# Performance work log

Measured on AMD Instinct MI355X. Metric: run time of the kernel, lower is better.

## Reference

```python
import math
import jax, jax.numpy as jnp
import numpy as np

B, L, S, H, E, D = 4, 2048, 2048, 8, 64, 64

def setup_inputs() -> dict:
    key = jax.random.key(0)
    kq, kk, kv = jax.random.split(key, 3)
    return {
        "queries": jax.random.normal(kq, (B, L, H, E), dtype=jnp.float32),
        "keys": jax.random.normal(kk, (B, S, H, E), dtype=jnp.float32),
        "values": jax.random.normal(kv, (B, S, H, D), dtype=jnp.float32),
    }

def reference(queries, keys, values):
    E_ = queries.shape[-1]
    scale = 1.0 / math.sqrt(E_)
    # scores: [B, H, L, S]
    scores = jnp.einsum('blhe,bshe->bhls', queries, keys)
    A = jax.nn.softmax(scale * scores, axis=-1)
    # dropout omitted (eval mode / p=0.0)
    out = jnp.einsum('bhls,bshd->blhd', A, values)
    return out
```

## Files before the change

### kernel.cpp

```cpp
#include <hip/hip_runtime.h>
#include <hip/hip_bf16.h>


#define BNUM 4
#define LLEN 2048
#define SLEN 2048
#define HNUM 8
#define EDIM 64

typedef __attribute__((ext_vector_type(8))) short bf16x8;
typedef __attribute__((ext_vector_type(4))) float f32x4;

__device__ __forceinline__ short f2bf(float f) {
    union { __hip_bfloat16 b; short s; } u;
    u.b = __float2bfloat16(f);
    return u.s;
}

#if __has_builtin(__builtin_amdgcn_global_load_lds)
#define HAVE_GLL 1
#else
#define HAVE_GLL 0
#endif

__device__ __forceinline__ void stage16(const short* g, short* l) {
#if HAVE_GLL
    __builtin_amdgcn_global_load_lds(
        (const __attribute__((address_space(1))) void*)g,
        (__attribute__((address_space(3))) void*)l, 16, 0, 0);
#else
    *(bf16x8*)l = *(const bf16x8*)g;
#endif
}

__global__ __launch_bounds__(256)
void prep(const float* __restrict__ Kg, const float* __restrict__ Vg,
          short* __restrict__ Kc, short* __restrict__ Vt)
{
    __shared__ short tile[EDIM][80];
    if (blockIdx.y == 0) {
        const int t = blockIdx.x * 256 + threadIdx.x;
        const int e8 = t & 7;
        const int tmp = t >> 3;
        const int h = tmp & 7;
        const int tmp2 = tmp >> 3;
        const int s = tmp2 & (SLEN - 1);
        const int b = tmp2 >> 11;
        const float4* src = (const float4*)(Kg + (((size_t)(b * SLEN + s) * HNUM + h) * EDIM + e8 * 8));
        float4 a = src[0], bb = src[1];
        bf16x8 o;
        o[0]=f2bf(a.x);  o[1]=f2bf(a.y);  o[2]=f2bf(a.z);  o[3]=f2bf(a.w);
        o[4]=f2bf(bb.x); o[5]=f2bf(bb.y); o[6]=f2bf(bb.z); o[7]=f2bf(bb.w);
        *(bf16x8*)(Kc + ((size_t)((b * HNUM + h) * SLEN + s) * EDIM + e8 * 8)) = o;
    } else {
        if (blockIdx.x >= 1024) return;
        const int x = blockIdx.x;
        const int s0 = (x & 31) * 64;
        const int bh = x >> 5;
        const int b = bh >> 3, h = bh & 7;
        {
            const int sr = threadIdx.x >> 2, dc = (threadIdx.x & 3) * 16;
            const float4* src = (const float4*)(Vg + (((size_t)(b * SLEN + s0 + sr) * HNUM + h) * EDIM + dc));
            #pragma unroll
            for (int j4 = 0; j4 < 4; ++j4) {
                float4 a = src[j4];
                tile[dc + j4*4 + 0][sr] = f2bf(a.x);
                tile[dc + j4*4 + 1][sr] = f2bf(a.y);
                tile[dc + j4*4 + 2][sr] = f2bf(a.z);
                tile[dc + j4*4 + 3][sr] = f2bf(a.w);
            }
        }
        __syncthreads();
        {
            const int dr = threadIdx.x >> 2, sc = (threadIdx.x & 3) * 16;
            short* dst = Vt + ((size_t)((b * HNUM + h) * EDIM + dr) * SLEN + s0 + sc);
            *(bf16x8*)dst       = *(const bf16x8*)&tile[dr][sc];
            *(bf16x8*)(dst + 8) = *(const bf16x8*)&tile[dr][sc + 8];
        }
    }
}

__global__ __launch_bounds__(256, 3)
void fa_fwd(const float* __restrict__ Qg, const short* __restrict__ Kc,
            const short* __restrict__ Vt, float* __restrict__ Og)
{
    __shared__ short sKV[16384];
    __shared__ float sL[4][64];

    const int tid  = threadIdx.x;
    const int wave = tid >> 6;
    const int lane = tid & 63;
    const int m    = lane & 15;
    const int quad = lane >> 4;
    const int h = blockIdx.y, b = blockIdx.z;
    const int qbase = blockIdx.x * 64;
    const int bh = b * HNUM + h;

    const short* Kbh = Kc + (size_t)bh * SLEN * EDIM;
    const short* Vbh = Vt + (size_t)bh * EDIM * SLEN;

    int ksrc[4], vsrc[4];
    short *kdst[4], *vdst[4];
    #pragma unroll
    for (int p = 0; p < 4; ++p) {
        const int krow = wave * 32 + p * 8 + (lane >> 3);
        const int kchk = (lane & 7) ^ ((p & 1) * 4 + ((lane >> 3) & 3));
        ksrc[p] = krow * EDIM + kchk * 8;
        kdst[p] = sKV + (wave * 256 + p * 64 + lane) * 8;
        const int vrow = p * 16 + (lane >> 2);
        const int vchk = (lane & 3) ^ ((lane >> 2) & 3);
        vsrc[p] = vrow * SLEN + wave * 32 + vchk * 8;
        vdst[p] = sKV + 8192 + (wave * 256 + p * 64 + lane) * 8;
    }

#define STAGE_TILE(s0)                                                  \
    do {                                                                \
        _Pragma("unroll")                                               \
        for (int p = 0; p < 4; ++p) {                                   \
            stage16(Kbh + (size_t)(s0) * EDIM + ksrc[p], kdst[p]);      \
            stage16(Vbh + (s0) + vsrc[p], vdst[p]);                     \
        }                                                               \
    } while (0)

    const float csc = 0.18033688011112042f;
    bf16x8 qfrag[4][2];
    #pragma unroll
    for (int qt = 0; qt < 4; ++qt)
        #pragma unroll
        for (int kb = 0; kb < 2; ++kb) {
            const float* qp = Qg + ((size_t)(b * LLEN + qbase + qt * 16 + m) * HNUM + h) * EDIM
                              + kb * 32 + quad * 8;
            float4 x0 = *(const float4*)qp;
            float4 x1 = *(const float4*)(qp + 4);
            bf16x8 f;
            f[0]=f2bf(x0.x*csc); f[1]=f2bf(x0.y*csc); f[2]=f2bf(x0.z*csc); f[3]=f2bf(x0.w*csc);
            f[4]=f2bf(x1.x*csc); f[5]=f2bf(x1.y*csc); f[6]=f2bf(x1.z*csc); f[7]=f2bf(x1.w*csc);
            qfrag[qt][kb] = f;
        }

    const int gk  = ((m >> 2) & 1) * 4 + (m & 3);
    const int pi0 = 8 * (m >> 2) + (m & 3);
    const int kOff00 = (wave * 32 + pi0)     * EDIM + ((quad)     ^ gk) * 8;
    const int kOff01 = (wave * 32 + pi0)     * EDIM + ((4 + quad) ^ gk) * 8;
    const int kOff10 = (wave * 32 + pi0 + 4) * EDIM + ((quad)     ^ gk) * 8;
    const int kOff11 = (wave * 32 + pi0 + 4) * EDIM + ((4 + quad) ^ gk) * 8;
    const int vOffB = 8192 + wave * 2048 + m * 32 + ((quad ^ (m & 3)) * 8);

    f32x4 oacc[4][4];
    #pragma unroll
    for (int i = 0; i < 4; ++i)
        #pragma unroll
        for (int j = 0; j < 4; ++j) oacc[i][j] = (f32x4){0.f, 0.f, 0.f, 0.f};
    float lsum[4] = {0.f, 0.f, 0.f, 0.f};

    STAGE_TILE(0);
    __syncthreads();

    for (int s0 = 0; s0 < SLEN; s0 += 128) {
        bf16x8 kf00 = *(const bf16x8*)(sKV + kOff00);
        bf16x8 kf01 = *(const bf16x8*)(sKV + kOff01);
        bf16x8 kf10 = *(const bf16x8*)(sKV + kOff10);
        bf16x8 kf11 = *(const bf16x8*)(sKV + kOff11);
        bf16x8 vf[4];
        #pragma unroll
        for (int dt = 0; dt < 4; ++dt)
            vf[dt] = *(const bf16x8*)(sKV + vOffB + dt * 512);

        __syncthreads();

        if (s0 + 128 < SLEN) STAGE_TILE(s0 + 128);

        #pragma unroll
        for (int qt = 0; qt < 4; ++qt) {
            f32x4 a0 = {0.f, 0.f, 0.f, 0.f};
            f32x4 a1 = {0.f, 0.f, 0.f, 0.f};
            a0 = __builtin_amdgcn_mfma_f32_16x16x32_bf16(kf00, qfrag[qt][0], a0, 0, 0, 0);
            a0 = __builtin_amdgcn_mfma_f32_16x16x32_bf16(kf01, qfrag[qt][1], a0, 0, 0, 0);
            a1 = __builtin_amdgcn_mfma_f32_16x16x32_bf16(kf10, qfrag[qt][0], a1, 0, 0, 0);
            a1 = __builtin_amdgcn_mfma_f32_16x16x32_bf16(kf11, qfrag[qt][1], a1, 0, 0, 0);
            float p0 = __builtin_amdgcn_exp2f(a0[0]);
            float p1 = __builtin_amdgcn_exp2f(a0[1]);
            float p2 = __builtin_amdgcn_exp2f(a0[2]);
            float p3 = __builtin_amdgcn_exp2f(a0[3]);
            float p4 = __builtin_amdgcn_exp2f(a1[0]);
            float p5 = __builtin_amdgcn_exp2f(a1[1]);
            float p6 = __builtin_amdgcn_exp2f(a1[2]);
            float p7 = __builtin_amdgcn_exp2f(a1[3]);
            lsum[qt] += ((p0 + p1) + (p2 + p3)) + ((p4 + p5) + (p6 + p7));
            bf16x8 pf;
            pf[0]=f2bf(p0); pf[1]=f2bf(p1); pf[2]=f2bf(p2); pf[3]=f2bf(p3);
            pf[4]=f2bf(p4); pf[5]=f2bf(p5); pf[6]=f2bf(p6); pf[7]=f2bf(p7);
            #pragma unroll
            for (int dt = 0; dt < 4; ++dt)
                oacc[qt][dt] = __builtin_amdgcn_mfma_f32_16x16x32_bf16(pf, vf[dt], oacc[qt][dt], 0, 0, 0);
        }

        __syncthreads();
    }

    #pragma unroll
    for (int qt = 0; qt < 4; ++qt) {
        float l = lsum[qt];
        l += __shfl_xor(l, 16);
        l += __shfl_xor(l, 32);
        if (lane < 16) sL[wave][qt * 16 + lane] = l;
    }
    __syncthreads();

    float* sO = (float*)sKV;
    for (int w = 0; w < 4; ++w) {
        if (wave == w) {
            #pragma unroll
            for (int qt = 0; qt < 4; ++qt)
                #pragma unroll
                for (int dt = 0; dt < 4; ++dt)
                    #pragma unroll
                    for (int r = 0; r < 4; ++r) {
                        const int q = qt * 16 + quad * 4 + r;
                        const int d = dt * 16 + m;
                        if (w == 0) sO[q * 64 + d] = oacc[qt][dt][r];
                        else        sO[q * 64 + d] += oacc[qt][dt][r];
                    }
        }
        __syncthreads();
    }

    {
        const int q = tid >> 2;
        const int dcol = (tid & 3) * 16;
        const float l = sL[0][q] + sL[1][q] + sL[2][q] + sL[3][q];
        const float inv = 1.0f / l;
        float* orow = Og + ((size_t)(b * LLEN + qbase + q) * HNUM + h) * EDIM + dcol;
        #pragma unroll
        for (int j = 0; j < 4; ++j) {
            float4 v = *(const float4*)(sO + q * 64 + dcol + j * 4);
            v.x *= inv; v.y *= inv; v.z *= inv; v.w *= inv;
            *(float4*)(orow + j * 4) = v;
        }
    }
}

extern "C" void kernel_launch(void* const* d_in, const int* in_sizes, int n_in,
                              void* d_out, int out_size, void* d_ws, size_t ws_size,
                              hipStream_t stream) {
    const float* Q = (const float*)d_in[0];
    const float* K = (const float*)d_in[1];
    const float* V = (const float*)d_in[2];
    float* O = (float*)d_out;

    const size_t NE = (size_t)BNUM * LLEN * HNUM * EDIM;
    short* Kc = (short*)d_ws;
    short* Vt = Kc + NE;

    prep<<<dim3(2048, 2), dim3(256), 0, stream>>>(K, V, Kc, Vt);
    fa_fwd<<<dim3(LLEN / 64, HNUM, BNUM), dim3(256), 0, stream>>>(Q, Kc, Vt, O);
}
```

Baseline: 153.0 us.

## Load K/V fragments directly from global memory instead of staging through LDS

Removes the global_load_lds staging of K and V tiles into shared memory and the per-tile barriers; each wave now reads its MFMA fragments straight from global (L2-cached) memory. Shared memory is reduced to a padded output-reduction buffer, which allows raising the launch-bound occupancy hint from 3 to 4 blocks. The padding of the output buffer row stride aims to reduce bank conflicts. The trade-off is less coalesced global loads and exposed global latency, with no explicit prefetch of the next tile.

```diff
diff --git a/kernel.cpp b/kernel.cpp
--- a/kernel.cpp
+++ b/kernel.cpp
@@ -15,22 +15,6 @@
     union { __hip_bfloat16 b; short s; } u;
     u.b = __float2bfloat16(f);
     return u.s;
-}
-
-#if __has_builtin(__builtin_amdgcn_global_load_lds)
-#define HAVE_GLL 1
-#else
-#define HAVE_GLL 0
-#endif
-
-__device__ __forceinline__ void stage16(const short* g, short* l) {
-#if HAVE_GLL
-    __builtin_amdgcn_global_load_lds(
-        (const __attribute__((address_space(1))) void*)g,
-        (__attribute__((address_space(3))) void*)l, 16, 0, 0);
-#else
-    *(bf16x8*)l = *(const bf16x8*)g;
-#endif
 }
 
 __global__ __launch_bounds__(256)
@@ -80,11 +64,11 @@
     }
 }
 
-__global__ __launch_bounds__(256, 3)
+__global__ __launch_bounds__(256, 4)
 void fa_fwd(const float* __restrict__ Qg, const short* __restrict__ Kc,
             const short* __restrict__ Vt, float* __restrict__ Og)
 {
-    __shared__ short sKV[16384];
+    __shared__ float sO[64 * 68];
     __shared__ float sL[4][64];
 
     const int tid  = threadIdx.x;
@@ -98,29 +82,6 @@
 
     const short* Kbh = Kc + (size_t)bh * SLEN * EDIM;
     const short* Vbh = Vt + (size_t)bh * EDIM * SLEN;
-
-    int ksrc[4], vsrc[4];
-    short *kdst[4], *vdst[4];
-    #pragma unroll
-    for (int p = 0; p < 4; ++p) {
-        const int krow = wave * 32 + p * 8 + (lane >> 3);
-        const int kchk = (lane & 7) ^ ((p & 1) * 4 + ((lane >> 3) & 3));
-        ksrc[p] = krow * EDIM + kchk * 8;
-        kdst[p] = sKV + (wave * 256 + p * 64 + lane) * 8;
-        const int vrow = p * 16 + (lane >> 2);
-        const int vchk = (lane & 3) ^ ((lane >> 2) & 3);
-        vsrc[p] = vrow * SLEN + wave * 32 + vchk * 8;
-        vdst[p] = sKV + 8192 + (wave * 256 + p * 64 + lane) * 8;
-    }
-
-#define STAGE_TILE(s0)                                                  \
-    do {                                                                \
-        _Pragma("unroll")                                               \
-        for (int p = 0; p < 4; ++p) {                                   \
-            stage16(Kbh + (size_t)(s0) * EDIM + ksrc[p], kdst[p]);      \
-            stage16(Vbh + (s0) + vsrc[p], vdst[p]);                     \
-        }                                                               \
-    } while (0)
 
     const float csc = 0.18033688011112042f;
     bf16x8 qfrag[4][2];
@@ -138,13 +99,10 @@
             qfrag[qt][kb] = f;
         }
 
-    const int gk  = ((m >> 2) & 1) * 4 + (m & 3);
     const int pi0 = 8 * (m >> 2) + (m & 3);
-    const int kOff00 = (wave * 32 + pi0)     * EDIM + ((quad)     ^ gk) * 8;
-    const int kOff01 = (wave * 32 + pi0)     * EDIM + ((4 + quad) ^ gk) * 8;
-    const int kOff10 = (wave * 32 + pi0 + 4) * EDIM + ((quad)     ^ gk) * 8;
-    const int kOff11 = (wave * 32 + pi0 + 4) * EDIM + ((4 + quad) ^ gk) * 8;
-    const int vOffB = 8192 + wave * 2048 + m * 32 + ((quad ^ (m & 3)) * 8);
+    const short* kp0 = Kbh + (size_t)(wave * 32 + pi0) * EDIM + quad * 8;
+    const short* kp1 = kp0 + 4 * EDIM;
+    const short* vp0 = Vbh + (size_t)m * SLEN + wave * 32 + quad * 8;
 
     f32x4 oacc[4][4];
     #pragma unroll
@@ -153,22 +111,18 @@
         for (int j = 0; j < 4; ++j) oacc[i][j] = (f32x4){0.f, 0.f, 0.f, 0.f};
     float lsum[4] = {0.f, 0.f, 0.f, 0.f};
 
-    STAGE_TILE(0);
-    __syncthreads();
-
     for (int s0 = 0; s0 < SLEN; s0 += 128) {
-        bf16x8 kf00 = *(const bf16x8*)(sKV + kOff00);
-        bf16x8 kf01 = *(const bf16x8*)(sKV + kOff01);
-        bf16x8 kf10 = *(const bf16x8*)(sKV + kOff10);
-        bf16x8 kf11 = *(const bf16x8*)(sKV + kOff11);
-        bf16x8 vf[4];
-        #pragma unroll
-        for (int dt = 0; dt < 4; ++dt)
-            vf[dt] = *(const bf16x8*)(sKV + vOffB + dt * 512);
-
-        __syncthreads();
-
-        if (s0 + 128 < SLEN) STAGE_TILE(s0 + 128);
+        const short* kp = kp0 + s0 * EDIM;
+        const short* kq = kp1 + s0 * EDIM;
+        bf16x8 kf00 = *(const bf16x8*)(kp);
+        bf16x8 kf01 = *(const bf16x8*)(kp + 32);
+        bf16x8 kf10 = *(const bf16x8*)(kq);
+        bf16x8 kf11 = *(const bf16x8*)(kq + 32);
+        const short* vp = vp0 + s0;
+        bf16x8 vf0 = *(const bf16x8*)(vp);
+        bf16x8 vf1 = *(const bf16x8*)(vp + 16 * SLEN);
+        bf16x8 vf2 = *(const bf16x8*)(vp + 32 * SLEN);
+        bf16x8 vf3 = *(const bf16x8*)(vp + 48 * SLEN);
 
         #pragma unroll
         for (int qt = 0; qt < 4; ++qt) {
@@ -190,12 +144,11 @@
             bf16x8 pf;
             pf[0]=f2bf(p0); pf[1]=f2bf(p1); pf[2]=f2bf(p2); pf[3]=f2bf(p3);
             pf[4]=f2bf(p4); pf[5]=f2bf(p5); pf[6]=f2bf(p6); pf[7]=f2bf(p7);
-            #pragma unroll
-            for (int dt = 0; dt < 4; ++dt)
-                oacc[qt][dt] = __builtin_amdgcn_mfma_f32_16x16x32_bf16(pf, vf[dt], oacc[qt][dt], 0, 0, 0);
-        }
-
-        __syncthreads();
+            oacc[qt][0] = __builtin_amdgcn_mfma_f32_16x16x32_bf16(pf, vf0, oacc[qt][0], 0, 0, 0);
+            oacc[qt][1] = __builtin_amdgcn_mfma_f32_16x16x32_bf16(pf, vf1, oacc[qt][1], 0, 0, 0);
+            oacc[qt][2] = __builtin_amdgcn_mfma_f32_16x16x32_bf16(pf, vf2, oacc[qt][2], 0, 0, 0);
+            oacc[qt][3] = __builtin_amdgcn_mfma_f32_16x16x32_bf16(pf, vf3, oacc[qt][3], 0, 0, 0);
+        }
     }
 
     #pragma unroll
@@ -207,7 +160,6 @@
     }
     __syncthreads();
 
-    float* sO = (float*)sKV;
     for (int w = 0; w < 4; ++w) {
         if (wave == w) {
             #pragma unroll
@@ -218,8 +170,8 @@
                     for (int r = 0; r < 4; ++r) {
                         const int q = qt * 16 + quad * 4 + r;
                         const int d = dt * 16 + m;
-                        if (w == 0) sO[q * 64 + d] = oacc[qt][dt][r];
-                        else        sO[q * 64 + d] += oacc[qt][dt][r];
+                        if (w == 0) sO[q * 68 + d] = oacc[qt][dt][r];
+                        else        sO[q * 68 + d] += oacc[qt][dt][r];
                     }
         }
         __syncthreads();
@@ -233,7 +185,7 @@
         float* orow = Og + ((size_t)(b * LLEN + qbase + q) * HNUM + h) * EDIM + dcol;
         #pragma unroll
         for (int j = 0; j < 4; ++j) {
-            float4 v = *(const float4*)(sO + q * 64 + dcol + j * 4);
+            float4 v = *(const float4*)(sO + q * 68 + dcol + j * 4);
             v.x *= inv; v.y *= inv; v.z *= inv; v.w *= inv;
             *(float4*)(orow + j * 4) = v;
         }
```

Measured after the change: 285.7 us. 1.87x slower.

## Shrink attention blocks to two waves with 32 queries and 64-key tiles

Applied to the files above, without the earlier changes.

Each block now has 128 threads instead of 256, handles 32 query rows instead of 64, and streams K/V in 64-key tiles, so the grid doubles to 2048 blocks. The cross-wave output reduction drops to two waves, and the shared output staging buffer gets a row stride of 68 floats to avoid bank conflicts. The aim is more resident blocks and less LDS per block, for better latency hiding and tail balance. In exchange, each staged K/V tile is reused by fewer queries, so K/V traffic doubles and there are more barriers per unit of matrix work.

```diff
diff --git a/kernel.cpp b/kernel.cpp
--- a/kernel.cpp
+++ b/kernel.cpp
@@ -80,12 +80,12 @@
     }
 }
 
-__global__ __launch_bounds__(256, 3)
+__global__ __launch_bounds__(128, 4)
 void fa_fwd(const float* __restrict__ Qg, const short* __restrict__ Kc,
             const short* __restrict__ Vt, float* __restrict__ Og)
 {
-    __shared__ short sKV[16384];
-    __shared__ float sL[4][64];
+    __shared__ short sKV[8192];
+    __shared__ float sL[2][32];
 
     const int tid  = threadIdx.x;
     const int wave = tid >> 6;
@@ -93,39 +93,33 @@
     const int m    = lane & 15;
     const int quad = lane >> 4;
     const int h = blockIdx.y, b = blockIdx.z;
-    const int qbase = blockIdx.x * 64;
+    const int qbase = blockIdx.x * 32;
     const int bh = b * HNUM + h;
 
     const short* Kbh = Kc + (size_t)bh * SLEN * EDIM;
     const short* Vbh = Vt + (size_t)bh * EDIM * SLEN;
 
-    int ksrc[4], vsrc[4];
-    short *kdst[4], *vdst[4];
+    const int l3 = lane >> 3;
+    const int ksrcE = (wave * 32 + l3) * EDIM + ((lane & 7) ^ (l3 & 3)) * 8;
+    const int ksrcO = (wave * 32 + l3) * EDIM + ((lane & 7) ^ (4 + (l3 & 3))) * 8;
+    const int vsrcB = (lane >> 2) * SLEN + wave * 32 + ((lane & 3) ^ ((lane >> 2) & 3)) * 8;
+    short* kdstB = sKV + (wave * 256 + lane) * 8;
+    short* vdstB = sKV + 4096 + (wave * 256 + lane) * 8;
+
+#define STAGE_TILE(s0)                                                        \
+    do {                                                                      \
+        _Pragma("unroll")                                                     \
+        for (int p = 0; p < 4; ++p) {                                         \
+            const int ks = ((p & 1) ? ksrcO : ksrcE) + (p >> 1) * 1024 + (p & 1) * 512; \
+            stage16(Kbh + (size_t)(s0) * EDIM + ks, kdstB + p * 512);         \
+            stage16(Vbh + (s0) + vsrcB + p * 16 * SLEN, vdstB + p * 512);     \
+        }                                                                     \
+    } while (0)
+
+    const float csc = 0.18033688011112042f;
+    bf16x8 qfrag[2][2];
     #pragma unroll
-    for (int p = 0; p < 4; ++p) {
-        const int krow = wave * 32 + p * 8 + (lane >> 3);
-        const int kchk = (lane & 7) ^ ((p & 1) * 4 + ((lane >> 3) & 3));
-        ksrc[p] = krow * EDIM + kchk * 8;
-        kdst[p] = sKV + (wave * 256 + p * 64 + lane) * 8;
-        const int vrow = p * 16 + (lane >> 2);
-        const int vchk = (lane & 3) ^ ((lane >> 2) & 3);
-        vsrc[p] = vrow * SLEN + wave * 32 + vchk * 8;
-        vdst[p] = sKV + 8192 + (wave * 256 + p * 64 + lane) * 8;
-    }
-
-#define STAGE_TILE(s0)                                                  \
-    do {                                                                \
-        _Pragma("unroll")                                               \
-        for (int p = 0; p < 4; ++p) {                                   \
-            stage16(Kbh + (size_t)(s0) * EDIM + ksrc[p], kdst[p]);      \
-            stage16(Vbh + (s0) + vsrc[p], vdst[p]);                     \
-        }                                                               \
-    } while (0)
-
-    const float csc = 0.18033688011112042f;
-    bf16x8 qfrag[4][2];
-    #pragma unroll
-    for (int qt = 0; qt < 4; ++qt)
+    for (int qt = 0; qt < 2; ++qt)
         #pragma unroll
         for (int kb = 0; kb < 2; ++kb) {
             const float* qp = Qg + ((size_t)(b * LLEN + qbase + qt * 16 + m) * HNUM + h) * EDIM
@@ -140,38 +134,38 @@
 
     const int gk  = ((m >> 2) & 1) * 4 + (m & 3);
     const int pi0 = 8 * (m >> 2) + (m & 3);
-    const int kOff00 = (wave * 32 + pi0)     * EDIM + ((quad)     ^ gk) * 8;
-    const int kOff01 = (wave * 32 + pi0)     * EDIM + ((4 + quad) ^ gk) * 8;
-    const int kOff10 = (wave * 32 + pi0 + 4) * EDIM + ((quad)     ^ gk) * 8;
-    const int kOff11 = (wave * 32 + pi0 + 4) * EDIM + ((4 + quad) ^ gk) * 8;
-    const int vOffB = 8192 + wave * 2048 + m * 32 + ((quad ^ (m & 3)) * 8);
-
-    f32x4 oacc[4][4];
+    const int kOff00 = (wave * 32 + pi0)     * 64 + ((quad)     ^ gk) * 8;
+    const int kOff01 = (wave * 32 + pi0)     * 64 + ((4 + quad) ^ gk) * 8;
+    const int kOff10 = (wave * 32 + pi0 + 4) * 64 + ((quad)     ^ gk) * 8;
+    const int kOff11 = (wave * 32 + pi0 + 4) * 64 + ((4 + quad) ^ gk) * 8;
+    const int vOffB  = 4096 + wave * 2048 + m * 32 + ((quad ^ (m & 3)) * 8);
+
+    f32x4 oacc[2][4];
     #pragma unroll
-    for (int i = 0; i < 4; ++i)
+    for (int i = 0; i < 2; ++i)
         #pragma unroll
         for (int j = 0; j < 4; ++j) oacc[i][j] = (f32x4){0.f, 0.f, 0.f, 0.f};
-    float lsum[4] = {0.f, 0.f, 0.f, 0.f};
+    float lsum[2] = {0.f, 0.f};
 
     STAGE_TILE(0);
     __syncthreads();
 
-    for (int s0 = 0; s0 < SLEN; s0 += 128) {
+    for (int s0 = 0; s0 < SLEN; s0 += 64) {
         bf16x8 kf00 = *(const bf16x8*)(sKV + kOff00);
         bf16x8 kf01 = *(const bf16x8*)(sKV + kOff01);
         bf16x8 kf10 = *(const bf16x8*)(sKV + kOff10);
         bf16x8 kf11 = *(const bf16x8*)(sKV + kOff11);
-        bf16x8 vf[4];
-        #pragma unroll
-        for (int dt = 0; dt < 4; ++dt)
-            vf[dt] = *(const bf16x8*)(sKV + vOffB + dt * 512);
+        bf16x8 vf0 = *(const bf16x8*)(sKV + vOffB);
+        bf16x8 vf1 = *(const bf16x8*)(sKV + vOffB + 512);
+        bf16x8 vf2 = *(const bf16x8*)(sKV + vOffB + 1024);
+        bf16x8 vf3 = *(const bf16x8*)(sKV + vOffB + 1536);
 
         __syncthreads();
 
-        if (s0 + 128 < SLEN) STAGE_TILE(s0 + 128);
-
-        #pragma unroll
-        for (int qt = 0; qt < 4; ++qt) {
+        if (s0 + 64 < SLEN) STAGE_TILE(s0 + 64);
+
+        #pragma unroll
+        for (int qt = 0; qt < 2; ++qt) {
             f32x4 a0 = {0.f, 0.f, 0.f, 0.f};
             f32x4 a1 = {0.f, 0.f, 0.f, 0.f};
             a0 = __builtin_amdgcn_mfma_f32_16x16x32_bf16(kf00, qfrag[qt][0], a0, 0, 0, 0);
@@ -190,16 +184,17 @@
             bf16x8 pf;
             pf[0]=f2bf(p0); pf[1]=f2bf(p1); pf[2]=f2bf(p2); pf[3]=f2bf(p3);
             pf[4]=f2bf(p4); pf[5]=f2bf(p5); pf[6]=f2bf(p6); pf[7]=f2bf(p7);
-            #pragma unroll
-            for (int dt = 0; dt < 4; ++dt)
-                oacc[qt][dt] = __builtin_amdgcn_mfma_f32_16x16x32_bf16(pf, vf[dt], oacc[qt][dt], 0, 0, 0);
+            oacc[qt][0] = __builtin_amdgcn_mfma_f32_16x16x32_bf16(pf, vf0, oacc[qt][0], 0, 0, 0);
+            oacc[qt][1] = __builtin_amdgcn_mfma_f32_16x16x32_bf16(pf, vf1, oacc[qt][1], 0, 0, 0);
+            oacc[qt][2] = __builtin_amdgcn_mfma_f32_16x16x32_bf16(pf, vf2, oacc[qt][2], 0, 0, 0);
+            oacc[qt][3] = __builtin_amdgcn_mfma_f32_16x16x32_bf16(pf, vf3, oacc[qt][3], 0, 0, 0);
         }
 
         __syncthreads();
     }
 
     #pragma unroll
-    for (int qt = 0; qt < 4; ++qt) {
+    for (int qt = 0; qt < 2; ++qt) {
         float l = lsum[qt];
         l += __shfl_xor(l, 16);
         l += __shfl_xor(l, 32);
@@ -208,32 +203,36 @@
     __syncthreads();
 
     float* sO = (float*)sKV;
-    for (int w = 0; w < 4; ++w) {
-        if (wave == w) {
+    if (wave == 0) {
+        #pragma unroll
+        for (int qt = 0; qt < 2; ++qt)
             #pragma unroll
-            for (int qt = 0; qt < 4; ++qt)
+            for (int dt = 0; dt < 4; ++dt)
                 #pragma unroll
-                for (int dt = 0; dt < 4; ++dt)
-                    #pragma unroll
-                    for (int r = 0; r < 4; ++r) {
-                        const int q = qt * 16 + quad * 4 + r;
-                        const int d = dt * 16 + m;
-                        if (w == 0) sO[q * 64 + d] = oacc[qt][dt][r];
-                        else        sO[q * 64 + d] += oacc[qt][dt][r];
-                    }
-        }
-        __syncthreads();
-    }
+                for (int r = 0; r < 4; ++r)
+                    sO[(qt * 16 + quad * 4 + r) * 68 + dt * 16 + m] = oacc[qt][dt][r];
+    }
+    __syncthreads();
+    if (wave == 1) {
+        #pragma unroll
+        for (int qt = 0; qt < 2; ++qt)
+            #pragma unroll
+            for (int dt = 0; dt < 4; ++dt)
+                #pragma unroll
+                for (int r = 0; r < 4; ++r)
+                    sO[(qt * 16 + quad * 4 + r) * 68 + dt * 16 + m] += oacc[qt][dt][r];
+    }
+    __syncthreads();
 
     {
         const int q = tid >> 2;
         const int dcol = (tid & 3) * 16;
-        const float l = sL[0][q] + sL[1][q] + sL[2][q] + sL[3][q];
+        const float l = sL[0][q] + sL[1][q];
         const float inv = 1.0f / l;
         float* orow = Og + ((size_t)(b * LLEN + qbase + q) * HNUM + h) * EDIM + dcol;
         #pragma unroll
         for (int j = 0; j < 4; ++j) {
-            float4 v = *(const float4*)(sO + q * 64 + dcol + j * 4);
+            float4 v = *(const float4*)(sO + q * 68 + dcol + j * 4);
             v.x *= inv; v.y *= inv; v.z *= inv; v.w *= inv;
             *(float4*)(orow + j * 4) = v;
         }
@@ -253,5 +252,5 @@
     short* Vt = Kc + NE;
 
     prep<<<dim3(2048, 2), dim3(256), 0, stream>>>(K, V, Kc, Vt);
-    fa_fwd<<<dim3(LLEN / 64, HNUM, BNUM), dim3(256), 0, stream>>>(Q, Kc, Vt, O);
-}
+    fa_fwd<<<dim3(LLEN / 32, HNUM, BNUM), dim3(128), 0, stream>>>(Q, Kc, Vt, O);
+}
```

Result: faster. 146.4 us (-4.3%).
